# Kernel optimization log

Hardware: AMD Instinct MI355X
Metric: run time of the kernel (lower is better)

Reference implementation:

```python
import jax, jax.numpy as jnp
import numpy as np

N, E, B = 100000, 1600000, 128
ND, ED, H, NC = 91, 20, 128, 3
EPS = 1e-5


def setup_inputs() -> dict:
    key = jax.random.key(0)
    ks = jax.random.split(key, 16)
    s = 0.05
    inp = {
        "node_feats": jax.random.normal(ks[0], (N, ND), jnp.float32),
        "edge_index": jax.random.randint(ks[1], (2, E), 0, N, dtype=jnp.int32),
        "edge_feats": jax.random.normal(ks[2], (E, ED), jnp.float32),
        "batch": jnp.sort(jax.random.randint(ks[3], (N,), 0, B, dtype=jnp.int32)),
        # params
        "embed_w": jax.random.normal(ks[4], (ND, H), jnp.float32) * s,
        "embed_b": jnp.zeros((H,), jnp.float32),
        "conv_wsrc": jax.random.normal(ks[5], (NC, H, 2 * H), jnp.float32) * s,
        "conv_wdst": jax.random.normal(ks[6], (NC, H, 2 * H), jnp.float32) * s,
        "conv_we": jax.random.normal(ks[7], (NC, ED, 2 * H), jnp.float32) * s,
        "conv_b": jnp.zeros((NC, 2 * H), jnp.float32),
        "bn_gamma": jnp.ones((NC, H), jnp.float32),
        "bn_beta": jnp.zeros((NC, H), jnp.float32),
        "fc1_w": jax.random.normal(ks[8], (H, H), jnp.float32) * s,
        "fc1_b": jnp.zeros((H,), jnp.float32),
        "fc_bn_gamma": jnp.ones((H,), jnp.float32),
        "fc_bn_beta": jnp.zeros((H,), jnp.float32),
        "out_w": jax.random.normal(ks[9], (H, 1), jnp.float32) * s,
        "out_b": jnp.zeros((1,), jnp.float32),
    }
    return inp


def _bn(x, gamma, beta):
    # training-mode batchnorm over axis 0, biased variance (torch semantics)
    m = x.mean(0)
    v = x.var(0)
    return (x - m) * jax.lax.rsqrt(v + EPS) * gamma + beta


def reference(node_feats, edge_index, edge_feats, batch, embed_w, embed_b,
              conv_wsrc, conv_wdst, conv_we, conv_b, bn_gamma, bn_beta,
              fc1_w, fc1_b, fc_bn_gamma, fc_bn_beta, out_w, out_b):
    h = node_feats @ embed_w + embed_b  # (N, H)
    src, dst = edge_index[0], edge_index[1]
    for i in range(NC):
        # CGCNN gated conv: Linear on concat[h_src, h_dst, e] split into 3 matmuls
        z = (h[src] @ conv_wsrc[i] + h[dst] @ conv_wdst[i]
             + edge_feats @ conv_we[i] + conv_b[i])  # (E, 2H)
        msg = jax.nn.sigmoid(z[:, :H]) * jax.nn.softplus(z[:, H:])
        agg = jax.ops.segment_sum(msg, dst, num_segments=N)  # (N, H)
        h = jax.nn.relu(h + _bn(agg, bn_gamma[i], bn_beta[i]))
    # global mean pool over graphs
    counts = jnp.maximum(
        jax.ops.segment_sum(jnp.ones((h.shape[0], 1), h.dtype), batch, num_segments=B), 1.0)
    g = jax.ops.segment_sum(h, batch, num_segments=B) / counts  # (B, H)
    x = jax.nn.relu(_bn(g @ fc1_w + fc1_b, fc_bn_gamma, fc_bn_beta))
    return x @ out_w + out_b  # (B, 1)
```

## Files before the change

### kernel.cpp

```cpp
#include <hip/hip_runtime.h>
#include <hip/hip_bf16.h>

#define NN 100000
#define EE 1600000
#define HH 128
#define NDIM 91
#define EDIM 20
#define BB 128
#define EPSF 1e-5f
#define NBLK 2048
#define PER 800
#define ECAP (NBLK * PER)
#define LN2I 1.44269504f

typedef __attribute__((ext_vector_type(8))) short short8v;
typedef __attribute__((ext_vector_type(4))) float f32x4;

__device__ __forceinline__ short f2bs(float x) {
  __hip_bfloat16 b = __float2bfloat16(x);
  return *reinterpret_cast<short*>(&b);
}
__device__ __forceinline__ float bl(unsigned int u) {
  union { unsigned int i; float f; } x; x.i = u << 16; return x.f;
}
__device__ __forceinline__ float bh(unsigned int u) {
  union { unsigned int i; float f; } x; x.i = u & 0xffff0000u; return x.f;
}

__global__ __launch_bounds__(256) void k_embed(const float* __restrict__ nf,
                                               const float* __restrict__ W,
                                               const float* __restrict__ b,
                                               float* __restrict__ h) {
  __shared__ float w_s[NDIM * HH];
  __shared__ float b_s[HH];
  __shared__ float a_s[16 * 92];
  for (int i = threadIdx.x; i < NDIM * HH; i += 256) w_s[i] = W[i];
  if (threadIdx.x < HH) b_s[threadIdx.x] = b[threadIdx.x];
  __syncthreads();
  int col = threadIdx.x & 127, rs = threadIdx.x >> 7;
  for (int base = blockIdx.x * 16; base < NN; base += gridDim.x * 16) {
    int nrows = min(16, NN - base);
    int tot = nrows * NDIM;
    for (int i = threadIdx.x; i < tot; i += 256) {
      int r = i / NDIM;
      a_s[r * 92 + (i - r * NDIM)] = nf[(size_t)base * NDIM + i];
    }
    __syncthreads();
    float acc[8];
#pragma unroll
    for (int r = 0; r < 8; r++) acc[r] = 0.f;
    for (int k = 0; k < NDIM; k++) {
      float w = w_s[k * HH + col];
#pragma unroll
      for (int r = 0; r < 8; r++) acc[r] += a_s[(rs * 8 + r) * 92 + k] * w;
    }
#pragma unroll
    for (int r = 0; r < 8; r++) {
      int row = base + rs * 8 + r;
      if (row < NN) h[(size_t)row * HH + col] = acc[r] + b_s[col];
    }
    __syncthreads();
  }
}

__global__ __launch_bounds__(256) void k_w2bf(const float* __restrict__ Wsrc,
                                              const float* __restrict__ Wdst,
                                              short* __restrict__ wt) {
  int i = blockIdx.x * 256 + threadIdx.x;
  if (i >= 2 * 256 * 128) return;
  int mat = i >> 15;
  int r = (i >> 7) & 255;
  int k = i & 127;
  const float* W = mat ? Wdst : Wsrc;
  wt[i] = f2bs(W[k * 256 + r]);
}

__global__ __launch_bounds__(256) void k_we2bf(const float* __restrict__ We,
                                               const float* __restrict__ bias,
                                               short* __restrict__ Web) {
  int i = blockIdx.x * 256 + threadIdx.x;
  if (i >= 256 * 32) return;
  int c = i >> 5, k = i & 31;
  float v = (k < EDIM) ? We[k * 256 + c] : (k == EDIM ? bias[c] : 0.f);
  float sc = (c < 128) ? -LN2I : LN2I;
  Web[i] = f2bs(v * sc);
}

__global__ __launch_bounds__(256) void k_node_mm(const float* __restrict__ h,
                                                 const short* __restrict__ wt,
                                                 unsigned int* __restrict__ hs2,
                                                 unsigned int* __restrict__ hd2) {
  __shared__ short hlds[64 * 128];
  int mat = blockIdx.y;
  const short* wtm = wt + mat * 256 * 128;
  unsigned int* out = mat ? hd2 : hs2;
  int base = blockIdx.x * 64;
  int t = threadIdx.x;
#pragma unroll
  for (int p = 0; p < 4; p++) {
    int e0 = (p * 256 + t) * 8;
    int row = e0 >> 7, col = e0 & 127;
    int gr = base + row;
    float4 f0 = make_float4(0.f, 0.f, 0.f, 0.f), f1 = f0;
    if (gr < NN) {
      f0 = *(const float4*)&h[(size_t)gr * 128 + col];
      f1 = *(const float4*)&h[(size_t)gr * 128 + col + 4];
    }
    short8v u;
    u[0] = f2bs(f0.x); u[1] = f2bs(f0.y); u[2] = f2bs(f0.z); u[3] = f2bs(f0.w);
    u[4] = f2bs(f1.x); u[5] = f2bs(f1.y); u[6] = f2bs(f1.z); u[7] = f2bs(f1.w);
    *(short8v*)&hlds[e0] = u;
  }
  __syncthreads();
  int w = t >> 6, l = t & 63;
  int cl = l & 15, kg = l >> 4;
  short8v a[4];
#pragma unroll
  for (int kk = 0; kk < 4; kk++)
    a[kk] = *(const short8v*)&hlds[(w * 16 + cl) * 128 + kk * 32 + kg * 8];
  f32x4 acc[16];
#pragma unroll
  for (int ct = 0; ct < 16; ct++) acc[ct] = (f32x4)(0.f);
#pragma unroll
  for (int ct = 0; ct < 16; ct++) {
#pragma unroll
    for (int kk = 0; kk < 4; kk++) {
      short8v b = *(const short8v*)&wtm[(ct * 16 + cl) * 128 + kk * 32 + kg * 8];
      acc[ct] = __builtin_amdgcn_mfma_f32_16x16x32_bf16(a[kk], b, acc[ct], 0, 0, 0);
    }
  }
#pragma unroll
  for (int ct = 0; ct < 8; ct++) {
#pragma unroll
    for (int r = 0; r < 4; r++) {
      int gr = base + w * 16 + kg * 4 + r;
      if (gr < NN) {
        unsigned short g = (unsigned short)f2bs(-LN2I * acc[ct][r]);
        unsigned short s = (unsigned short)f2bs(LN2I * acc[ct + 8][r]);
        out[(size_t)gr * 128 + ct * 16 + cl] =
            (unsigned int)g | ((unsigned int)s << 16);
      }
    }
  }
}

__global__ __launch_bounds__(256) void k_hist(const int* __restrict__ dst,
                                              int* __restrict__ cnt) {
  for (int e = blockIdx.x * 256 + threadIdx.x; e < EE; e += gridDim.x * 256)
    atomicAdd(&cnt[dst[e]], 1);
}

__global__ __launch_bounds__(1024) void k_scan(const int* __restrict__ cnt,
                                               int* __restrict__ off) {
  __shared__ int ps[1024];
  int t = threadIdx.x;
  const int R = (NN + 1023) / 1024;
  int b0 = t * R, b1 = min(NN, b0 + R);
  int s = 0;
  for (int i = b0; i < b1; i++) s += cnt[i];
  ps[t] = s;
  __syncthreads();
  for (int d = 1; d < 1024; d <<= 1) {
    int v = (t >= d) ? ps[t - d] : 0;
    __syncthreads();
    ps[t] += v;
    __syncthreads();
  }
  int run = (t == 0) ? 0 : ps[t - 1];
  for (int i = b0; i < b1; i++) {
    off[i] = run;
    run += cnt[i];
  }
}

__global__ __launch_bounds__(256) void k_scatter(const int* __restrict__ src,
                                                 const int* __restrict__ dst,
                                                 const float* __restrict__ ef,
                                                 int* __restrict__ off,
                                                 int* __restrict__ src_s,
                                                 int* __restrict__ dst_s,
                                                 short* __restrict__ efp) {
  for (int e = blockIdx.x * 256 + threadIdx.x; e < EE; e += gridDim.x * 256) {
    int d = dst[e];
    int pos = atomicAdd(&off[d], 1);
    src_s[pos] = src[e];
    dst_s[pos] = d;
    const float4* in = (const float4*)&ef[(size_t)e * EDIM];
    float4 q0 = in[0], q1 = in[1], q2 = in[2], q3 = in[3], q4 = in[4];
    short8v u0, u1, u2, u3;
    u0[0] = f2bs(q0.x); u0[1] = f2bs(q0.y); u0[2] = f2bs(q0.z); u0[3] = f2bs(q0.w);
    u0[4] = f2bs(q1.x); u0[5] = f2bs(q1.y); u0[6] = f2bs(q1.z); u0[7] = f2bs(q1.w);
    u1[0] = f2bs(q2.x); u1[1] = f2bs(q2.y); u1[2] = f2bs(q2.z); u1[3] = f2bs(q2.w);
    u1[4] = f2bs(q3.x); u1[5] = f2bs(q3.y); u1[6] = f2bs(q3.z); u1[7] = f2bs(q3.w);
    u2[0] = f2bs(q4.x); u2[1] = f2bs(q4.y); u2[2] = f2bs(q4.z); u2[3] = f2bs(q4.w);
    u2[4] = f2bs(1.0f); u2[5] = 0; u2[6] = 0; u2[7] = 0;
    u3 = (short8v)(short)0;
    short8v* op = (short8v*)&efp[(size_t)pos * 32];
    op[0] = u0; op[1] = u1; op[2] = u2; op[3] = u3;
  }
}

__global__ __launch_bounds__(256) void k_padtail(int* __restrict__ src_s,
                                                 int* __restrict__ dst_s,
                                                 short* __restrict__ efp) {
  int e = EE + blockIdx.x * 256 + threadIdx.x;
  if (e >= ECAP) return;
  src_s[e] = 0;
  dst_s[e] = -2;
  short8v z = (short8v)(short)0;
  short8v* op = (short8v*)&efp[(size_t)e * 32];
  op[0] = z; op[1] = z; op[2] = z; op[3] = z;
}

__global__ __launch_bounds__(256) void k_edge_v5(
    const unsigned int* __restrict__ hs2, const unsigned int* __restrict__ hd2,
    const short* __restrict__ efp, const int* __restrict__ srcp,
    const int* __restrict__ dstp, const short* __restrict__ Web,
    float* __restrict__ agg) {
  const int i0 = blockIdx.x * PER;
  int t = threadIdx.x;
  int w = t >> 6, l = t & 63, cl = l & 15, kg = l >> 4;
  int c0 = w * 32 + cl, c1 = c0 + 16;
  short8v bg0 = *(const short8v*)&Web[c0 * 32 + kg * 8];
  short8v bg1 = *(const short8v*)&Web[c1 * 32 + kg * 8];
  short8v bs0 = *(const short8v*)&Web[(128 + c0) * 32 + kg * 8];
  short8v bs1 = *(const short8v*)&Web[(128 + c1) * 32 + kg * 8];
  int cur = -1;
  float acc0 = 0.f, acc1 = 0.f;
  float hg0 = 0.f, hp0 = 0.f, hg1 = 0.f, hp1 = 0.f;
  const int o_a_base = i0 + (cl >> 2) * 200 + (cl & 3);
  const int o_e_base = i0 + kg * 200;
  for (int it = 0; it < 50; ++it) {
    int off4 = it * 4;
    short8v a = *(const short8v*)&efp[(o_a_base + off4) * 32 + kg * 8];
    f32x4 zgv0 = __builtin_amdgcn_mfma_f32_16x16x32_bf16(a, bg0, (f32x4)(0.f), 0, 0, 0);
    f32x4 zgv1 = __builtin_amdgcn_mfma_f32_16x16x32_bf16(a, bg1, (f32x4)(0.f), 0, 0, 0);
    f32x4 zsv0 = __builtin_amdgcn_mfma_f32_16x16x32_bf16(a, bs0, (f32x4)(0.f), 0, 0, 0);
    f32x4 zsv1 = __builtin_amdgcn_mfma_f32_16x16x32_bf16(a, bs1, (f32x4)(0.f), 0, 0, 0);
    int o_e = o_e_base + off4;
#pragma unroll
    for (int r = 0; r < 4; ++r) {
      int o = o_e + r;
      int s = srcp[o];
      int d = dstp[o];
      if (d != cur) {
        if (cur >= 0) {
          atomicAdd(&agg[cur * HH + c0], acc0);
          atomicAdd(&agg[cur * HH + c1], acc1);
        }
        acc0 = 0.f; acc1 = 0.f;
        cur = d;
        if (d >= 0) {
          unsigned int x0 = hd2[(d << 7) + c0];
          unsigned int x1 = hd2[(d << 7) + c1];
          hg0 = bl(x0); hp0 = bh(x0);
          hg1 = bl(x1); hp1 = bh(x1);
        }
      }
      unsigned int u0 = hs2[(s << 7) + c0];
      unsigned int u1 = hs2[(s << 7) + c1];
      float zgN0 = zgv0[r] + bl(u0) + hg0;
      float zsp0 = zsv0[r] + bh(u0) + hp0;
      float zgN1 = zgv1[r] + bl(u1) + hg1;
      float zsp1 = zsv1[r] + bh(u1) + hp1;
      float sp0 = __builtin_amdgcn_logf(1.f + __builtin_amdgcn_exp2f(zsp0));
      float sp1 = __builtin_amdgcn_logf(1.f + __builtin_amdgcn_exp2f(zsp1));
      acc0 += sp0 * __builtin_amdgcn_rcpf(1.f + __builtin_amdgcn_exp2f(zgN0));
      acc1 += sp1 * __builtin_amdgcn_rcpf(1.f + __builtin_amdgcn_exp2f(zgN1));
    }
  }
  if (cur >= 0) {
    atomicAdd(&agg[cur * HH + c0], acc0);
    atomicAdd(&agg[cur * HH + c1], acc1);
  }
}

__global__ __launch_bounds__(256) void k_bn_stats(const float* __restrict__ agg,
                                                  float* __restrict__ stats) {
  int col = threadIdx.x & 127, hlf = threadIdx.x >> 7;
  float s = 0.f, sq = 0.f;
  for (int row = blockIdx.x * 2 + hlf; row < NN; row += gridDim.x * 2) {
    float v = agg[(size_t)row * HH + col];
    s += v; sq += v * v;
  }
  __shared__ float ls[256], lq[256];
  ls[threadIdx.x] = s; lq[threadIdx.x] = sq;
  __syncthreads();
  if (hlf == 0) {
    atomicAdd(&stats[col], ls[col] + ls[col + 128]);
    atomicAdd(&stats[128 + col], lq[col] + lq[col + 128]);
  }
}

__global__ void k_bn_fin(float* stats, const float* __restrict__ gam,
                         const float* __restrict__ bet) {
  int c = threadIdx.x;
  if (c >= HH) return;
  float mean = stats[c] / (float)NN;
  float var = stats[HH + c] / (float)NN - mean * mean;
  float sc = rsqrtf(var + EPSF) * gam[c];
  stats[c] = sc;
  stats[HH + c] = bet[c] - mean * sc;
}

__global__ __launch_bounds__(256) void k_update(float* __restrict__ h,
                                                const float* __restrict__ agg,
                                                const float* __restrict__ stats) {
  for (size_t i = (size_t)blockIdx.x * blockDim.x + threadIdx.x; i < (size_t)NN * HH;
       i += (size_t)gridDim.x * blockDim.x) {
    int c = (int)(i & 127);
    float v = h[i] + agg[i] * stats[c] + stats[128 + c];
    h[i] = fmaxf(v, 0.f);
  }
}

__global__ void k_pool(const float* __restrict__ h, const int* __restrict__ batch,
                       float* __restrict__ g, float* __restrict__ gcnt) {
  int col = threadIdx.x;
  int chunk = (NN + gridDim.x - 1) / gridDim.x;
  int n0 = blockIdx.x * chunk, n1 = min(NN, n0 + chunk);
  if (n0 >= n1) return;
  int cur = batch[n0];
  float acc = 0.f, cnt = 0.f;
  for (int n = n0; n < n1; n++) {
    int bb = batch[n];
    if (bb != cur) {
      atomicAdd(&g[cur * HH + col], acc);
      if (col == 0) atomicAdd(&gcnt[cur], cnt);
      acc = 0.f; cnt = 0.f; cur = bb;
    }
    acc += h[(size_t)n * HH + col];
    cnt += 1.f;
  }
  atomicAdd(&g[cur * HH + col], acc);
  if (col == 0) atomicAdd(&gcnt[cur], cnt);
}

__global__ __launch_bounds__(256) void k_final(float* __restrict__ g,
                                               const float* __restrict__ gcnt,
                                               const float* __restrict__ fc1w,
                                               const float* __restrict__ fc1b,
                                               const float* __restrict__ gam,
                                               const float* __restrict__ bet,
                                               const float* __restrict__ ow,
                                               const float* __restrict__ ob,
                                               float* __restrict__ out) {
  __shared__ float w_s[HH * HH];
  __shared__ float y_s[BB * HH];
  __shared__ float ls[256], lq[256];
  for (int i = threadIdx.x; i < HH * HH; i += 256) w_s[i] = fc1w[i];
  for (int i = threadIdx.x; i < BB * HH; i += 256) {
    int r = i >> 7;
    g[i] = g[i] / fmaxf(gcnt[r], 1.f);
  }
  __syncthreads();
  int c = threadIdx.x & 127, h2 = threadIdx.x >> 7;
  for (int rr = 0; rr < 64; rr++) {
    int r = h2 * 64 + rr;
    float acc = fc1b[c];
    for (int k = 0; k < HH; k++) acc += g[r * HH + k] * w_s[k * HH + c];
    y_s[r * HH + c] = acc;
  }
  __syncthreads();
  float s = 0.f, sq = 0.f;
  for (int rr = 0; rr < 64; rr++) {
    float v = y_s[(h2 * 64 + rr) * HH + c];
    s += v; sq += v * v;
  }
  ls[threadIdx.x] = s; lq[threadIdx.x] = sq;
  __syncthreads();
  if (h2 == 0) {
    float ss = ls[c] + ls[c + 128], qq = lq[c] + lq[c + 128];
    float mean = ss / (float)BB, var = qq / (float)BB - mean * mean;
    float sc = rsqrtf(var + EPSF) * gam[c];
    ls[c] = sc;
    lq[c] = bet[c] - mean * sc;
  }
  __syncthreads();
  for (int rr = 0; rr < 64; rr++) {
    int r = h2 * 64 + rr;
    y_s[r * HH + c] = fmaxf(y_s[r * HH + c] * ls[c] + lq[c], 0.f);
  }
  __syncthreads();
  int r2 = threadIdx.x >> 1, hf = threadIdx.x & 1;
  float acc = 0.f;
  for (int k = hf * 64; k < hf * 64 + 64; k++) acc += y_s[r2 * HH + k] * ow[k];
  __syncthreads();
  ls[threadIdx.x] = acc;
  __syncthreads();
  if (hf == 0) out[r2] = ls[threadIdx.x] + ls[threadIdx.x + 1] + ob[0];
}

extern "C" void kernel_launch(void* const* d_in, const int* in_sizes, int n_in,
                              void* d_out, int out_size, void* d_ws, size_t ws_size,
                              hipStream_t stream) {
  (void)in_sizes; (void)n_in; (void)out_size; (void)ws_size;
  const float* node_feats = (const float*)d_in[0];
  const int* edge_index = (const int*)d_in[1];
  const float* edge_feats = (const float*)d_in[2];
  const int* batch = (const int*)d_in[3];
  const float* embed_w = (const float*)d_in[4];
  const float* embed_b = (const float*)d_in[5];
  const float* conv_wsrc = (const float*)d_in[6];
  const float* conv_wdst = (const float*)d_in[7];
  const float* conv_we = (const float*)d_in[8];
  const float* conv_b = (const float*)d_in[9];
  const float* bn_gamma = (const float*)d_in[10];
  const float* bn_beta = (const float*)d_in[11];
  const float* fc1_w = (const float*)d_in[12];
  const float* fc1_b = (const float*)d_in[13];
  const float* fc_bn_gamma = (const float*)d_in[14];
  const float* fc_bn_beta = (const float*)d_in[15];
  const float* out_w = (const float*)d_in[16];
  const float* out_b = (const float*)d_in[17];

  char* ws = (char*)d_ws;
  size_t o = 0;
  float* h = (float*)(ws + o);              o += (size_t)NN * HH * 4;
  unsigned int* hs2 = (unsigned int*)(ws + o); o += (size_t)NN * 128 * 4;
  unsigned int* hd2 = (unsigned int*)(ws + o); o += (size_t)NN * 128 * 4;
  float* agg = (float*)(ws + o);            o += (size_t)NN * HH * 4;
  short* efp = (short*)(ws + o);            o += (size_t)ECAP * 32 * 2;
  int* src_s = (int*)(ws + o);              o += (size_t)ECAP * 4;
  int* dst_s = (int*)(ws + o);              o += (size_t)ECAP * 4;
  int* cnt = (int*)(ws + o);                o += (size_t)NN * 4;
  int* off = (int*)(ws + o);                o += (size_t)NN * 4;
  short* wt = (short*)(ws + o);             o += (size_t)2 * 256 * 128 * 2;
  short* Web = (short*)(ws + o);            o += (size_t)256 * 32 * 2;
  float* stats = (float*)(ws + o);          o += 256 * 4;
  float* g = (float*)(ws + o);              o += (size_t)BB * HH * 4;
  float* gcnt = (float*)(ws + o);           o += BB * 4;

  const int* src = edge_index;
  const int* dst = edge_index + EE;

  hipMemsetAsync(cnt, 0, (size_t)NN * 4, stream);
  k_hist<<<2048, 256, 0, stream>>>(dst, cnt);
  k_scan<<<1, 1024, 0, stream>>>(cnt, off);
  k_scatter<<<2048, 256, 0, stream>>>(src, dst, edge_feats, off, src_s, dst_s, efp);
  k_padtail<<<(ECAP - EE + 255) / 256, 256, 0, stream>>>(src_s, dst_s, efp);

  k_embed<<<512, 256, 0, stream>>>(node_feats, embed_w, embed_b, h);

  for (int i = 0; i < 3; i++) {
    k_w2bf<<<256, 256, 0, stream>>>(conv_wsrc + (size_t)i * HH * 256,
                                    conv_wdst + (size_t)i * HH * 256, wt);
    k_we2bf<<<32, 256, 0, stream>>>(conv_we + (size_t)i * EDIM * 256,
                                    conv_b + (size_t)i * 256, Web);
    k_node_mm<<<dim3((NN + 63) / 64, 2), 256, 0, stream>>>(h, wt, hs2, hd2);
    hipMemsetAsync(agg, 0, (size_t)NN * HH * 4, stream);
    hipMemsetAsync(stats, 0, 256 * 4, stream);
    k_edge_v5<<<NBLK, 256, 0, stream>>>(hs2, hd2, efp, src_s, dst_s, Web, agg);
    k_bn_stats<<<1024, 256, 0, stream>>>(agg, stats);
    k_bn_fin<<<1, 128, 0, stream>>>(stats, bn_gamma + i * HH, bn_beta + i * HH);
    k_update<<<2048, 256, 0, stream>>>(h, agg, stats);
  }

  hipMemsetAsync(g, 0, (size_t)BB * HH * 4, stream);
  hipMemsetAsync(gcnt, 0, BB * 4, stream);
  k_pool<<<256, 128, 0, stream>>>(h, batch, g, gcnt);
  k_final<<<1, 256, 0, stream>>>(g, gcnt, fc1_w, fc1_b, fc_bn_gamma, fc_bn_beta,
                                 out_w, out_b, (float*)d_out);
}
```

Before: 2.128 ms.

## Fuse BN update into node matmul, vectorize edge gathers, halve edge chunk size

The BN-apply/residual/ReLU update for layers 1 and 2 moves into the node matmul kernel, which now computes both src and dst projections in one block from a single staged h tile, saving an h read pass and an update kernel per layer. The hs2/hd2 output columns are interleaved so each edge thread fetches its two channels with one 64-bit load, and src/dst indices are read as int4. Edge blocks double in number while each handles half as many edges, shortening the per-block serial loop at the cost of more boundary atomics. The final update runs once after the loop.

```diff
diff --git a/kernel.cpp b/kernel.cpp
--- a/kernel.cpp
+++ b/kernel.cpp
@@ -8,8 +8,8 @@
 #define EDIM 20
 #define BB 128
 #define EPSF 1e-5f
-#define NBLK 2048
-#define PER 800
+#define NBLK 4096
+#define PER 400
 #define ECAP (NBLK * PER)
 #define LN2I 1.44269504f
 
@@ -86,16 +86,21 @@
   Web[i] = f2bs(v * sc);
 }
 
-__global__ __launch_bounds__(256) void k_node_mm(const float* __restrict__ h,
+__global__ __launch_bounds__(256) void k_node_mm(float* __restrict__ h,
+                                                 const float* __restrict__ agg,
+                                                 const float* __restrict__ stats,
                                                  const short* __restrict__ wt,
                                                  unsigned int* __restrict__ hs2,
-                                                 unsigned int* __restrict__ hd2) {
+                                                 unsigned int* __restrict__ hd2,
+                                                 int apply) {
   __shared__ short hlds[64 * 128];
-  int mat = blockIdx.y;
-  const short* wtm = wt + mat * 256 * 128;
-  unsigned int* out = mat ? hd2 : hs2;
+  __shared__ float st_s[256];
   int base = blockIdx.x * 64;
   int t = threadIdx.x;
+  if (apply) {
+    if (t < 256) st_s[t] = stats[t];
+    __syncthreads();
+  }
 #pragma unroll
   for (int p = 0; p < 4; p++) {
     int e0 = (p * 256 + t) * 8;
@@ -105,6 +110,20 @@
     if (gr < NN) {
       f0 = *(const float4*)&h[(size_t)gr * 128 + col];
       f1 = *(const float4*)&h[(size_t)gr * 128 + col + 4];
+      if (apply) {
+        float4 a0 = *(const float4*)&agg[(size_t)gr * 128 + col];
+        float4 a1 = *(const float4*)&agg[(size_t)gr * 128 + col + 4];
+        f0.x = fmaxf(f0.x + a0.x * st_s[col] + st_s[128 + col], 0.f);
+        f0.y = fmaxf(f0.y + a0.y * st_s[col + 1] + st_s[129 + col], 0.f);
+        f0.z = fmaxf(f0.z + a0.z * st_s[col + 2] + st_s[130 + col], 0.f);
+        f0.w = fmaxf(f0.w + a0.w * st_s[col + 3] + st_s[131 + col], 0.f);
+        f1.x = fmaxf(f1.x + a1.x * st_s[col + 4] + st_s[132 + col], 0.f);
+        f1.y = fmaxf(f1.y + a1.y * st_s[col + 5] + st_s[133 + col], 0.f);
+        f1.z = fmaxf(f1.z + a1.z * st_s[col + 6] + st_s[134 + col], 0.f);
+        f1.w = fmaxf(f1.w + a1.w * st_s[col + 7] + st_s[135 + col], 0.f);
+        *(float4*)&h[(size_t)gr * 128 + col] = f0;
+        *(float4*)&h[(size_t)gr * 128 + col + 4] = f1;
+      }
     }
     short8v u;
     u[0] = f2bs(f0.x); u[1] = f2bs(f0.y); u[2] = f2bs(f0.z); u[3] = f2bs(f0.w);
@@ -118,27 +137,32 @@
 #pragma unroll
   for (int kk = 0; kk < 4; kk++)
     a[kk] = *(const short8v*)&hlds[(w * 16 + cl) * 128 + kk * 32 + kg * 8];
-  f32x4 acc[16];
-#pragma unroll
-  for (int ct = 0; ct < 16; ct++) acc[ct] = (f32x4)(0.f);
-#pragma unroll
-  for (int ct = 0; ct < 16; ct++) {
-#pragma unroll
-    for (int kk = 0; kk < 4; kk++) {
-      short8v b = *(const short8v*)&wtm[(ct * 16 + cl) * 128 + kk * 32 + kg * 8];
-      acc[ct] = __builtin_amdgcn_mfma_f32_16x16x32_bf16(a[kk], b, acc[ct], 0, 0, 0);
-    }
-  }
-#pragma unroll
-  for (int ct = 0; ct < 8; ct++) {
-#pragma unroll
-    for (int r = 0; r < 4; r++) {
-      int gr = base + w * 16 + kg * 4 + r;
-      if (gr < NN) {
-        unsigned short g = (unsigned short)f2bs(-LN2I * acc[ct][r]);
-        unsigned short s = (unsigned short)f2bs(LN2I * acc[ct + 8][r]);
-        out[(size_t)gr * 128 + ct * 16 + cl] =
-            (unsigned int)g | ((unsigned int)s << 16);
+#pragma unroll
+  for (int mat = 0; mat < 2; mat++) {
+    const short* wtm = wt + mat * 256 * 128;
+    unsigned int* out = mat ? hd2 : hs2;
+    f32x4 acc[16];
+#pragma unroll
+    for (int ct = 0; ct < 16; ct++) acc[ct] = (f32x4)(0.f);
+#pragma unroll
+    for (int ct = 0; ct < 16; ct++) {
+#pragma unroll
+      for (int kk = 0; kk < 4; kk++) {
+        short8v b = *(const short8v*)&wtm[(ct * 16 + cl) * 128 + kk * 32 + kg * 8];
+        acc[ct] = __builtin_amdgcn_mfma_f32_16x16x32_bf16(a[kk], b, acc[ct], 0, 0, 0);
+      }
+    }
+#pragma unroll
+    for (int ct = 0; ct < 8; ct++) {
+#pragma unroll
+      for (int r = 0; r < 4; r++) {
+        int gr = base + w * 16 + kg * 4 + r;
+        if (gr < NN) {
+          unsigned short g = (unsigned short)f2bs(-LN2I * acc[ct][r]);
+          unsigned short s = (unsigned short)f2bs(LN2I * acc[ct + 8][r]);
+          int slot = (ct >> 1) * 32 + (cl << 1) + (ct & 1);
+          out[(size_t)gr * 128 + slot] = (unsigned int)g | ((unsigned int)s << 16);
+        }
       }
     }
   }
@@ -212,7 +236,7 @@
   op[0] = z; op[1] = z; op[2] = z; op[3] = z;
 }
 
-__global__ __launch_bounds__(256) void k_edge_v5(
+__global__ __launch_bounds__(256) void k_edge_v6(
     const unsigned int* __restrict__ hs2, const unsigned int* __restrict__ hd2,
     const short* __restrict__ efp, const int* __restrict__ srcp,
     const int* __restrict__ dstp, const short* __restrict__ Web,
@@ -221,6 +245,7 @@
   int t = threadIdx.x;
   int w = t >> 6, l = t & 63, cl = l & 15, kg = l >> 4;
   int c0 = w * 32 + cl, c1 = c0 + 16;
+  int pairoff = w * 32 + (cl << 1);
   short8v bg0 = *(const short8v*)&Web[c0 * 32 + kg * 8];
   short8v bg1 = *(const short8v*)&Web[c1 * 32 + kg * 8];
   short8v bs0 = *(const short8v*)&Web[(128 + c0) * 32 + kg * 8];
@@ -228,21 +253,23 @@
   int cur = -1;
   float acc0 = 0.f, acc1 = 0.f;
   float hg0 = 0.f, hp0 = 0.f, hg1 = 0.f, hp1 = 0.f;
-  const int o_a_base = i0 + (cl >> 2) * 200 + (cl & 3);
-  const int o_e_base = i0 + kg * 200;
-  for (int it = 0; it < 50; ++it) {
+  const int o_a_base = i0 + (cl >> 2) * 100 + (cl & 3);
+  const int o_e_base = i0 + kg * 100;
+  for (int it = 0; it < 25; ++it) {
     int off4 = it * 4;
-    short8v a = *(const short8v*)&efp[(o_a_base + off4) * 32 + kg * 8];
+    short8v a = *(const short8v*)&efp[(size_t)(o_a_base + off4) * 32 + kg * 8];
     f32x4 zgv0 = __builtin_amdgcn_mfma_f32_16x16x32_bf16(a, bg0, (f32x4)(0.f), 0, 0, 0);
     f32x4 zgv1 = __builtin_amdgcn_mfma_f32_16x16x32_bf16(a, bg1, (f32x4)(0.f), 0, 0, 0);
     f32x4 zsv0 = __builtin_amdgcn_mfma_f32_16x16x32_bf16(a, bs0, (f32x4)(0.f), 0, 0, 0);
     f32x4 zsv1 = __builtin_amdgcn_mfma_f32_16x16x32_bf16(a, bs1, (f32x4)(0.f), 0, 0, 0);
     int o_e = o_e_base + off4;
+    int4 s4 = *(const int4*)&srcp[o_e];
+    int4 d4 = *(const int4*)&dstp[o_e];
+    int ss[4] = {s4.x, s4.y, s4.z, s4.w};
+    int dd[4] = {d4.x, d4.y, d4.z, d4.w};
 #pragma unroll
     for (int r = 0; r < 4; ++r) {
-      int o = o_e + r;
-      int s = srcp[o];
-      int d = dstp[o];
+      int s = ss[r], d = dd[r];
       if (d != cur) {
         if (cur >= 0) {
           atomicAdd(&agg[cur * HH + c0], acc0);
@@ -251,18 +278,16 @@
         acc0 = 0.f; acc1 = 0.f;
         cur = d;
         if (d >= 0) {
-          unsigned int x0 = hd2[(d << 7) + c0];
-          unsigned int x1 = hd2[(d << 7) + c1];
-          hg0 = bl(x0); hp0 = bh(x0);
-          hg1 = bl(x1); hp1 = bh(x1);
+          uint2 x = *(const uint2*)&hd2[((size_t)d << 7) + pairoff];
+          hg0 = bl(x.x); hp0 = bh(x.x);
+          hg1 = bl(x.y); hp1 = bh(x.y);
         }
       }
-      unsigned int u0 = hs2[(s << 7) + c0];
-      unsigned int u1 = hs2[(s << 7) + c1];
-      float zgN0 = zgv0[r] + bl(u0) + hg0;
-      float zsp0 = zsv0[r] + bh(u0) + hp0;
-      float zgN1 = zgv1[r] + bl(u1) + hg1;
-      float zsp1 = zsv1[r] + bh(u1) + hp1;
+      uint2 u = *(const uint2*)&hs2[((size_t)s << 7) + pairoff];
+      float zgN0 = zgv0[r] + bl(u.x) + hg0;
+      float zsp0 = zsv0[r] + bh(u.x) + hp0;
+      float zgN1 = zgv1[r] + bl(u.y) + hg1;
+      float zsp1 = zsv1[r] + bh(u.y) + hp1;
       float sp0 = __builtin_amdgcn_logf(1.f + __builtin_amdgcn_exp2f(zsp0));
       float sp1 = __builtin_amdgcn_logf(1.f + __builtin_amdgcn_exp2f(zsp1));
       acc0 += sp0 * __builtin_amdgcn_rcpf(1.f + __builtin_amdgcn_exp2f(zgN0));
@@ -447,14 +472,15 @@
                                     conv_wdst + (size_t)i * HH * 256, wt);
     k_we2bf<<<32, 256, 0, stream>>>(conv_we + (size_t)i * EDIM * 256,
                                     conv_b + (size_t)i * 256, Web);
-    k_node_mm<<<dim3((NN + 63) / 64, 2), 256, 0, stream>>>(h, wt, hs2, hd2);
+    k_node_mm<<<(NN + 63) / 64, 256, 0, stream>>>(h, agg, stats, wt, hs2, hd2,
+                                                  i > 0 ? 1 : 0);
     hipMemsetAsync(agg, 0, (size_t)NN * HH * 4, stream);
     hipMemsetAsync(stats, 0, 256 * 4, stream);
-    k_edge_v5<<<NBLK, 256, 0, stream>>>(hs2, hd2, efp, src_s, dst_s, Web, agg);
+    k_edge_v6<<<NBLK, 256, 0, stream>>>(hs2, hd2, efp, src_s, dst_s, Web, agg);
     k_bn_stats<<<1024, 256, 0, stream>>>(agg, stats);
     k_bn_fin<<<1, 128, 0, stream>>>(stats, bn_gamma + i * HH, bn_beta + i * HH);
-    k_update<<<2048, 256, 0, stream>>>(h, agg, stats);
-  }
+  }
+  k_update<<<2048, 256, 0, stream>>>(h, agg, stats);
 
   hipMemsetAsync(g, 0, (size_t)BB * HH * 4, stream);
   hipMemsetAsync(gcnt, 0, BB * 4, stream);
```

After: 2.033 ms. -4.4%, faster.
